# Optimization experiments

Hardware: AMD Instinct MI355X
Metric: run time of the kernel (lower is better)

## Reference

```python
import jax, jax.numpy as jnp
import numpy as np

B, S, D, N = 4, 4096, 512, 512  # d_state must equal d_model for the original broadcast to be valid


def setup_inputs() -> dict:
    key = jax.random.key(0)
    ks = jax.random.split(key, 8)
    inv = 1.0 / np.sqrt(D)
    return {
        "x": jax.random.normal(ks[0], (B, S, D), dtype=jnp.float32),
        "state0": jnp.zeros((B, N), dtype=jnp.float32),
        "W_gate": (jax.random.normal(ks[1], (D, D)) * inv).astype(jnp.float32),  # x_proj_gate.weight [out,in]
        "b_gate": jnp.zeros((D,), jnp.float32),
        "W_sp": (jax.random.normal(ks[2], (N, D)) * inv).astype(jnp.float32),    # state_proj.weight [d_state, d_model]
        "b_sp": jnp.zeros((N,), jnp.float32),
        "W_out": (jax.random.normal(ks[3], (D, D)) * inv).astype(jnp.float32),   # out_proj.weight
        "b_out": jnp.zeros((D,), jnp.float32),
        "A_log": (jax.random.normal(ks[4], (D, N)) * 0.02).astype(jnp.float32),
        "D_param": jnp.ones((D,), jnp.float32),
    }


def reference(x, state0, W_gate, b_gate, W_sp, b_sp, W_out, b_out, A_log, D_param):
    # x_gate = silu(x_proj_gate(x))  [B,S,D]
    x_gate = jax.nn.silu(x @ W_gate.T + b_gate)
    # s = state_proj(x_gate)  [B,S,N]
    s = x_gate @ W_sp.T + b_sp
    # A = -exp(A_log); per-step decay = exp(mean_N(A))  [D] (== N by construction)
    A = -jnp.exp(A_log)
    decay = jnp.exp(A.mean(axis=-1))

    def step(state, s_t):  # state [B,N], s_t [B,N]
        state = state * decay + s_t
        return state, state

    state_f, states = jax.lax.scan(step, state0, jnp.swapaxes(s, 0, 1))  # states [S,B,N]
    # y_t = state_t @ state_proj.weight + D * u_t
    y = jnp.einsum('sbn,nd->bsd', states, W_sp) + D_param * x_gate
    out = y @ W_out.T + b_out  # out_proj
    return out, state_f
```

## Files before the change

### kernel.cpp

```cpp
#include <hip/hip_runtime.h>
#include <hip/hip_bf16.h>
#include <stdint.h>


typedef __bf16 bf16_t;
typedef bf16_t bf16x8 __attribute__((ext_vector_type(8)));
typedef bf16_t bf16x4 __attribute__((ext_vector_type(4)));
typedef float  f32x4  __attribute__((ext_vector_type(4)));

static __device__ __forceinline__ void async_copy16(bf16_t* lds, const bf16_t* g) {
    __builtin_amdgcn_global_load_lds((const __attribute__((address_space(1))) void*)g,
                                     (__attribute__((address_space(3))) void*)lds, 16, 0, 0);
}

template <int MODE, int NT, bool SCAN, bool F32A>
static __device__ __forceinline__ void gemm_body(
    int bid, int nwg, bf16_t* __restrict__ AsB, bf16_t* __restrict__ BsB,
    const void* __restrict__ A0v, const bf16_t* __restrict__ W0,
    const bf16_t* __restrict__ A1, const bf16_t* __restrict__ W1,
    const float* __restrict__ bias, void* __restrict__ outp,
    const float* __restrict__ decay_g, float* __restrict__ carry_g)
{
    constexpr int K = 512;
    const int tid = threadIdx.x;
    if ((nwg & 7) == 0) bid = (bid & 7) * (nwg >> 3) + (bid >> 3);
    const int m0 = (bid >> 2) << 7, n0 = (bid & 3) << 7;
    const int l = tid & 63, w = tid >> 6;
    const int wr = w >> 2, wc = w & 3;
    const int lr = l & 15, kc = l >> 4;
    const int rloc = l >> 3, sc = (l & 7) ^ rloc;

    float bv[2];
    #pragma unroll
    for (int j = 0; j < 2; ++j)
        bv[j] = bias ? bias[n0 + wc * 32 + j * 16 + lr] : 0.f;

    f32x4 acc[4][2];
    const f32x4 z = {0.f, 0.f, 0.f, 0.f};
    #pragma unroll
    for (int i = 0; i < 4; ++i)
        #pragma unroll
        for (int j = 0; j < 2; ++j) acc[i][j] = z;

    const bf16_t* __restrict__ A0b = (const bf16_t*)A0v;
    const float*  __restrict__ A0f = (const float*)A0v;
    const int arow = tid >> 2, aq = tid & 3;

    auto stage = [&](int t) {
        const bf16_t* __restrict__ Asrc = (t < 8) ? A0b : A1;
        const bf16_t* __restrict__ Wsrc = (t < 8) ? W0 : W1;
        const int kk = (t & 7) << 6;
        bf16_t* bufA = AsB + (t & 1) * 8192;
        bf16_t* bufB = BsB + (t & 1) * 8192;
        #pragma unroll
        for (int v = 0; v < 2; ++v) {
            const int win = w * 2 + v;
            async_copy16(bufA + win * 512,
                         Asrc + (size_t)(m0 + win * 8 + rloc) * K + kk + sc * 8);
            async_copy16(bufB + win * 512,
                         Wsrc + (size_t)(n0 + win * 8 + rloc) * K + kk + sc * 8);
        }
    };
    auto stageB = [&](int t) {
        const int kk = (t & 7) << 6;
        bf16_t* bufB = BsB + (t & 1) * 8192;
        #pragma unroll
        for (int v = 0; v < 2; ++v) {
            const int win = w * 2 + v;
            async_copy16(bufB + win * 512,
                         W0 + (size_t)(n0 + win * 8 + rloc) * K + kk + sc * 8);
        }
    };
    float4 arA[4];
    auto issueA = [&](int t) {
        const float* p = A0f + (size_t)(m0 + arow) * K + ((t & 7) << 6) + aq * 16;
        arA[0] = ((const float4*)p)[0];
        arA[1] = ((const float4*)p)[1];
        arA[2] = ((const float4*)p)[2];
        arA[3] = ((const float4*)p)[3];
    };
    auto writeA = [&](int t) {
        bf16x8 v0, v1;
        v0[0]=(bf16_t)arA[0].x; v0[1]=(bf16_t)arA[0].y; v0[2]=(bf16_t)arA[0].z; v0[3]=(bf16_t)arA[0].w;
        v0[4]=(bf16_t)arA[1].x; v0[5]=(bf16_t)arA[1].y; v0[6]=(bf16_t)arA[1].z; v0[7]=(bf16_t)arA[1].w;
        v1[0]=(bf16_t)arA[2].x; v1[1]=(bf16_t)arA[2].y; v1[2]=(bf16_t)arA[2].z; v1[3]=(bf16_t)arA[2].w;
        v1[4]=(bf16_t)arA[3].x; v1[5]=(bf16_t)arA[3].y; v1[6]=(bf16_t)arA[3].z; v1[7]=(bf16_t)arA[3].w;
        bf16_t* bufA = AsB + (t & 1) * 8192;
        *(bf16x8*)(bufA + arow * 64 + (((aq * 2    ) ^ (arow & 7)) << 3)) = v0;
        *(bf16x8*)(bufA + arow * 64 + (((aq * 2 + 1) ^ (arow & 7)) << 3)) = v1;
    };

    if (F32A) { issueA(0); asm volatile("" ::: "memory"); stageB(0); }
    else      { stage(0); }

    #pragma unroll
    for (int t = 0; t < NT; ++t) {
        if (F32A) {
            asm volatile("s_waitcnt vmcnt(2)" ::: "memory");
            writeA(t);
            if (t + 1 < NT) {
                issueA(t + 1);
                asm volatile("" ::: "memory");
                stageB(t + 1);
                asm volatile("s_waitcnt vmcnt(6) lgkmcnt(0)" ::: "memory");
            } else {
                asm volatile("s_waitcnt vmcnt(0) lgkmcnt(0)" ::: "memory");
            }
        } else {
            if (t + 1 < NT) {
                stage(t + 1);
                asm volatile("s_waitcnt vmcnt(4)" ::: "memory");
            } else {
                asm volatile("s_waitcnt vmcnt(0)" ::: "memory");
            }
        }
        __builtin_amdgcn_s_barrier();
        const bf16_t* __restrict__ bufA = AsB + (t & 1) * 8192;
        const bf16_t* __restrict__ bufB = BsB + (t & 1) * 8192;
        bf16x8 a[2][4], b[2][2];
        #pragma unroll
        for (int ks = 0; ks < 2; ++ks) {
            #pragma unroll
            for (int i = 0; i < 4; ++i)
                a[ks][i] = *(const bf16x8*)(bufA + (wr * 64 + i * 16 + lr) * 64
                                            + (((ks * 4 + kc) ^ (lr & 7)) << 3));
            #pragma unroll
            for (int j = 0; j < 2; ++j)
                b[ks][j] = *(const bf16x8*)(bufB + (wc * 32 + j * 16 + lr) * 64
                                            + (((ks * 4 + kc) ^ (lr & 7)) << 3));
        }
        #pragma unroll
        for (int ks = 0; ks < 2; ++ks)
            #pragma unroll
            for (int i = 0; i < 4; ++i)
                #pragma unroll
                for (int j = 0; j < 2; ++j)
                    acc[i][j] = __builtin_amdgcn_mfma_f32_16x16x32_bf16(
                        a[ks][i], b[ks][j], acc[i][j], 0, 0, 0);
        if (t + 1 < NT)
            __builtin_amdgcn_s_barrier();
    }

    if (MODE == 0) {
        float* outF = (float*)outp;
        #pragma unroll
        for (int i = 0; i < 4; ++i) {
            const int row = m0 + wr * 64 + i * 16 + kc * 4;
            #pragma unroll
            for (int j = 0; j < 2; ++j) {
                const int col = n0 + wc * 32 + j * 16 + lr;
                #pragma unroll
                for (int r = 0; r < 4; ++r)
                    outF[(size_t)(row + r) * 512 + col] = acc[i][j][r] + bv[j];
            }
        }
    } else {
        __syncthreads();
        bf16_t* eps = AsB;
        #pragma unroll
        for (int i = 0; i < 4; ++i) {
            const int row = wr * 64 + i * 16 + kc * 4;
            #pragma unroll
            for (int j = 0; j < 2; ++j) {
                const int col = wc * 32 + j * 16 + lr;
                #pragma unroll
                for (int r = 0; r < 4; ++r) {
                    float v = acc[i][j][r] + bv[j];
                    if (MODE == 2) v = v / (1.f + __expf(-v));
                    eps[(row + r) * 128 + col] = (bf16_t)v;
                }
            }
        }
        __syncthreads();
        bf16_t* outB = (bf16_t*)outp;
        #pragma unroll
        for (int s2 = 0; s2 < 4; ++s2) {
            const int row = s2 * 32 + (tid >> 4);
            const int col = (tid & 15) * 8;
            *(bf16x8*)(outB + (size_t)(m0 + row) * 512 + n0 + col) =
                *(const bf16x8*)(eps + row * 128 + col);
        }
        if (SCAN) {
            const int sub = tid >> 7, col = tid & 127;
            const int n = n0 + col;
            const float dec = decay_g[n];
            float st = 0.f;
            #pragma unroll 8
            for (int i = 0; i < 32; ++i)
                st = st * dec + (float)eps[(sub * 32 + i) * 128 + col];
            carry_g[(size_t)((m0 >> 5) + sub) * 512 + n] = st;
        }
    }
}

template <int MODE, int NT, bool SCAN, bool F32A>
__global__ __launch_bounds__(512, 4) void gemm_std(
    const void* __restrict__ A0v, const bf16_t* __restrict__ W0,
    const bf16_t* __restrict__ A1, const bf16_t* __restrict__ W1,
    const float* __restrict__ bias, void* __restrict__ outp,
    const float* __restrict__ decay_g, float* __restrict__ carry_g)
{
    __shared__ bf16_t As[2 * 128 * 64];
    __shared__ bf16_t Bs[2 * 128 * 64];
    gemm_body<MODE, NT, SCAN, F32A>(blockIdx.x, gridDim.x, As, Bs,
                                    A0v, W0, A1, W1, bias, outp, decay_g, carry_g);
}

__global__ __launch_bounds__(512, 4) void g1_wct(
    const float* __restrict__ x, const bf16_t* __restrict__ Wg,
    const float* __restrict__ b_gate, bf16_t* __restrict__ xg,
    const bf16_t* __restrict__ Wo, const bf16_t* __restrict__ Wsp,
    bf16_t* __restrict__ WcT)
{
    __shared__ bf16_t As[2 * 128 * 64];
    __shared__ bf16_t Bs[2 * 128 * 64];
    if (blockIdx.x < 512)
        gemm_body<2, 8, false, true>(blockIdx.x, 512, As, Bs,
            (const void*)x, Wg, (const bf16_t*)nullptr, (const bf16_t*)nullptr,
            b_gate, (void*)xg, (const float*)nullptr, (float*)nullptr);
    else
        gemm_body<1, 8, false, false>(blockIdx.x - 512, 16, As, Bs,
            (const void*)Wo, Wsp, (const bf16_t*)nullptr, (const bf16_t*)nullptr,
            (const float*)nullptr, (void*)WcT, (const float*)nullptr, (float*)nullptr);
}

__global__ void prep_all(const float* __restrict__ Wg, const float* __restrict__ Wsp,
                         const float* __restrict__ Wo, const float* __restrict__ Dp,
                         bf16_t* __restrict__ Wg_bf, bf16_t* __restrict__ Wsp_bf,
                         bf16_t* __restrict__ Wo_bf, bf16_t* __restrict__ W2_bf,
                         const float* __restrict__ A_log, float* __restrict__ decay)
{
    const int blk = blockIdx.x, tid = threadIdx.x;
    {
        int i = blk * 256 + tid;
        Wg_bf[i]  = (bf16_t)Wg[i];
        Wsp_bf[i] = (bf16_t)Wsp[i];
        float wo  = Wo[i];
        Wo_bf[i]  = (bf16_t)wo;
        W2_bf[i]  = (bf16_t)(wo * Dp[i & 511]);
    }
    if (blk < 128) {
        int d = blk * 4 + (tid >> 6);
        int ll = tid & 63;
        const float* row = A_log + (size_t)d * 512;
        float s = 0.f;
        for (int k = ll; k < 512; k += 64) s += expf(row[k]);
        #pragma unroll
        for (int off = 32; off > 0; off >>= 1) s += __shfl_down(s, off);
        if (ll == 0) decay[d] = expf(-s * (1.f / 512.f));
    }
}

__global__ void scan_carry(float* __restrict__ carry, const float* __restrict__ decay,
                           const float* __restrict__ state0, float* __restrict__ state_f)
{
    int g = blockIdx.x * 256 + threadIdx.x;
    int n = g & 511, b = g >> 9;
    float dec = decay[n];
    float d32 = dec;
    #pragma unroll
    for (int t = 0; t < 5; ++t) d32 *= d32;
    float st = state0[g];
    for (int ch = 0; ch < 128; ++ch) {
        size_t idx = (size_t)(b * 128 + ch) * 512 + n;
        float c = carry[idx];
        carry[idx] = st;
        st = st * d32 + c;
    }
    state_f[g] = st;
}

__global__ void scan_final8(const bf16_t* __restrict__ s, const float* __restrict__ decay,
                            const float* __restrict__ exc, bf16_t* __restrict__ states)
{
    int g = blockIdx.x * 128 + threadIdx.x;
    int ng = g & 63, ch = (g >> 6) & 127, b = g >> 13;
    const int n0 = ng * 8;
    float4 d0 = *(const float4*)(decay + n0);
    float4 d1 = *(const float4*)(decay + n0 + 4);
    const float* ep = exc + (size_t)(b * 128 + ch) * 512 + n0;
    float4 s0 = *(const float4*)ep;
    float4 s1 = *(const float4*)(ep + 4);
    float st[8] = {s0.x, s0.y, s0.z, s0.w, s1.x, s1.y, s1.z, s1.w};
    const float dc[8] = {d0.x, d0.y, d0.z, d0.w, d1.x, d1.y, d1.z, d1.w};
    size_t base = (size_t)(b * 4096 + ch * 32) * 512 + n0;
    #pragma unroll 8
    for (int i = 0; i < 32; ++i) {
        bf16x8 v = *(const bf16x8*)(s + base + (size_t)i * 512);
        bf16x8 o;
        #pragma unroll
        for (int k = 0; k < 8; ++k) {
            st[k] = st[k] * dc[k] + (float)v[k];
            o[k] = (bf16_t)st[k];
        }
        *(bf16x8*)(states + base + (size_t)i * 512) = o;
    }
}

extern "C" void kernel_launch(void* const* d_in, const int* in_sizes, int n_in,
                              void* d_out, int out_size, void* d_ws, size_t ws_size,
                              hipStream_t stream)
{
    const float* x      = (const float*)d_in[0];
    const float* state0 = (const float*)d_in[1];
    const float* W_gate = (const float*)d_in[2];
    const float* b_gate = (const float*)d_in[3];
    const float* W_sp   = (const float*)d_in[4];
    const float* b_sp   = (const float*)d_in[5];
    const float* W_out  = (const float*)d_in[6];
    const float* b_out  = (const float*)d_in[7];
    const float* A_log  = (const float*)d_in[8];
    const float* D_par  = (const float*)d_in[9];
    float* out = (float*)d_out;

    char* ws = (char*)d_ws;
    bf16_t* states = (bf16_t*)ws;
    bf16_t* xg_bf  = (bf16_t*)(ws + (16u << 20));
    bf16_t* s_bf   = (bf16_t*)(ws + (32u << 20));
    bf16_t* Wg_bf  = (bf16_t*)(ws + (48u << 20));
    bf16_t* Wsp_bf = Wg_bf + 262144;
    bf16_t* Wo_bf  = Wg_bf + 2 * 262144;
    bf16_t* W2_bf  = Wg_bf + 3 * 262144;
    bf16_t* WcT_bf = Wg_bf + 4 * 262144;
    float*  carry  = (float*)(Wg_bf + 5 * 262144);
    float*  decay  = carry + 262144;

    prep_all<<<dim3(1024), dim3(256), 0, stream>>>(
        W_gate, W_sp, W_out, D_par, Wg_bf, Wsp_bf, Wo_bf, W2_bf, A_log, decay);

    g1_wct<<<dim3(528), dim3(512), 0, stream>>>(
        x, Wg_bf, b_gate, xg_bf, Wo_bf, Wsp_bf, WcT_bf);

    gemm_std<1, 8, true, false><<<dim3(512), dim3(512), 0, stream>>>(
        (const void*)xg_bf, Wsp_bf, (const bf16_t*)nullptr, (const bf16_t*)nullptr,
        b_sp, (void*)s_bf, decay, carry);

    scan_carry<<<dim3(8), dim3(256), 0, stream>>>(carry, decay, state0, out + 8388608);
    scan_final8<<<dim3(256), dim3(128), 0, stream>>>(s_bf, decay, carry, states);

    gemm_std<0, 16, false, false><<<dim3(512), dim3(512), 0, stream>>>(
        (const void*)states, WcT_bf, xg_bf, W2_bf, b_out, (void*)out,
        (const float*)nullptr, (float*)nullptr);
}
```

Baseline: 83.44 us.

## Deepen GEMM shared-memory pipeline to triple buffering with prefetch distance two

Switches the LDS A/B tiles from double to triple buffering and issues global loads two k-tiles ahead instead of one, with the vmcnt waits adjusted to match. For the fp32-A path it double-buffers the register staging of x. The aim is to hide more global memory latency behind the MFMA work. In exchange LDS per block rises from 64KB to 96KB and the launch bound drops from 4 to 2 blocks per CU, which lowers occupancy and adds register pressure.

```diff
diff --git a/kernel.cpp b/kernel.cpp
--- a/kernel.cpp
+++ b/kernel.cpp
@@ -50,8 +50,8 @@
         const bf16_t* __restrict__ Asrc = (t < 8) ? A0b : A1;
         const bf16_t* __restrict__ Wsrc = (t < 8) ? W0 : W1;
         const int kk = (t & 7) << 6;
-        bf16_t* bufA = AsB + (t & 1) * 8192;
-        bf16_t* bufB = BsB + (t & 1) * 8192;
+        bf16_t* bufA = AsB + (t % 3) * 8192;
+        bf16_t* bufB = BsB + (t % 3) * 8192;
         #pragma unroll
         for (int v = 0; v < 2; ++v) {
             const int win = w * 2 + v;
@@ -63,7 +63,7 @@
     };
     auto stageB = [&](int t) {
         const int kk = (t & 7) << 6;
-        bf16_t* bufB = BsB + (t & 1) * 8192;
+        bf16_t* bufB = BsB + (t % 3) * 8192;
         #pragma unroll
         for (int v = 0; v < 2; ++v) {
             const int win = w * 2 + v;
@@ -71,52 +71,51 @@
                          W0 + (size_t)(n0 + win * 8 + rloc) * K + kk + sc * 8);
         }
     };
-    float4 arA[4];
+    float4 arA[2][4];
     auto issueA = [&](int t) {
         const float* p = A0f + (size_t)(m0 + arow) * K + ((t & 7) << 6) + aq * 16;
-        arA[0] = ((const float4*)p)[0];
-        arA[1] = ((const float4*)p)[1];
-        arA[2] = ((const float4*)p)[2];
-        arA[3] = ((const float4*)p)[3];
+        arA[t & 1][0] = ((const float4*)p)[0];
+        arA[t & 1][1] = ((const float4*)p)[1];
+        arA[t & 1][2] = ((const float4*)p)[2];
+        arA[t & 1][3] = ((const float4*)p)[3];
     };
     auto writeA = [&](int t) {
+        const float4* ar = arA[t & 1];
         bf16x8 v0, v1;
-        v0[0]=(bf16_t)arA[0].x; v0[1]=(bf16_t)arA[0].y; v0[2]=(bf16_t)arA[0].z; v0[3]=(bf16_t)arA[0].w;
-        v0[4]=(bf16_t)arA[1].x; v0[5]=(bf16_t)arA[1].y; v0[6]=(bf16_t)arA[1].z; v0[7]=(bf16_t)arA[1].w;
-        v1[0]=(bf16_t)arA[2].x; v1[1]=(bf16_t)arA[2].y; v1[2]=(bf16_t)arA[2].z; v1[3]=(bf16_t)arA[2].w;
-        v1[4]=(bf16_t)arA[3].x; v1[5]=(bf16_t)arA[3].y; v1[6]=(bf16_t)arA[3].z; v1[7]=(bf16_t)arA[3].w;
-        bf16_t* bufA = AsB + (t & 1) * 8192;
+        v0[0]=(bf16_t)ar[0].x; v0[1]=(bf16_t)ar[0].y; v0[2]=(bf16_t)ar[0].z; v0[3]=(bf16_t)ar[0].w;
+        v0[4]=(bf16_t)ar[1].x; v0[5]=(bf16_t)ar[1].y; v0[6]=(bf16_t)ar[1].z; v0[7]=(bf16_t)ar[1].w;
+        v1[0]=(bf16_t)ar[2].x; v1[1]=(bf16_t)ar[2].y; v1[2]=(bf16_t)ar[2].z; v1[3]=(bf16_t)ar[2].w;
+        v1[4]=(bf16_t)ar[3].x; v1[5]=(bf16_t)ar[3].y; v1[6]=(bf16_t)ar[3].z; v1[7]=(bf16_t)ar[3].w;
+        bf16_t* bufA = AsB + (t % 3) * 8192;
         *(bf16x8*)(bufA + arow * 64 + (((aq * 2    ) ^ (arow & 7)) << 3)) = v0;
         *(bf16x8*)(bufA + arow * 64 + (((aq * 2 + 1) ^ (arow & 7)) << 3)) = v1;
     };
 
-    if (F32A) { issueA(0); asm volatile("" ::: "memory"); stageB(0); }
-    else      { stage(0); }
+    if (F32A) { issueA(0); asm volatile("" ::: "memory"); stageB(0);
+                issueA(1); asm volatile("" ::: "memory"); stageB(1); }
+    else      { stage(0); stage(1); }
 
     #pragma unroll
     for (int t = 0; t < NT; ++t) {
         if (F32A) {
-            asm volatile("s_waitcnt vmcnt(2)" ::: "memory");
+            if (t + 1 < NT) asm volatile("s_waitcnt vmcnt(6)" ::: "memory");
+            else            asm volatile("s_waitcnt vmcnt(0)" ::: "memory");
             writeA(t);
-            if (t + 1 < NT) {
-                issueA(t + 1);
+            if (t + 2 < NT) {
+                issueA(t + 2);
                 asm volatile("" ::: "memory");
-                stageB(t + 1);
-                asm volatile("s_waitcnt vmcnt(6) lgkmcnt(0)" ::: "memory");
-            } else {
-                asm volatile("s_waitcnt vmcnt(0) lgkmcnt(0)" ::: "memory");
+                stageB(t + 2);
             }
+            asm volatile("s_waitcnt lgkmcnt(0)" ::: "memory");
         } else {
-            if (t + 1 < NT) {
-                stage(t + 1);
-                asm volatile("s_waitcnt vmcnt(4)" ::: "memory");
-            } else {
-                asm volatile("s_waitcnt vmcnt(0)" ::: "memory");
-            }
+            if (t + 2 < NT) stage(t + 2);
+            if (t + 2 < NT)      asm volatile("s_waitcnt vmcnt(8)" ::: "memory");
+            else if (t + 1 < NT) asm volatile("s_waitcnt vmcnt(4)" ::: "memory");
+            else                 asm volatile("s_waitcnt vmcnt(0)" ::: "memory");
         }
         __builtin_amdgcn_s_barrier();
-        const bf16_t* __restrict__ bufA = AsB + (t & 1) * 8192;
-        const bf16_t* __restrict__ bufB = BsB + (t & 1) * 8192;
+        const bf16_t* __restrict__ bufA = AsB + (t % 3) * 8192;
+        const bf16_t* __restrict__ bufB = BsB + (t % 3) * 8192;
         bf16x8 a[2][4], b[2][2];
         #pragma unroll
         for (int ks = 0; ks < 2; ++ks) {
@@ -194,26 +193,26 @@
 }
 
 template <int MODE, int NT, bool SCAN, bool F32A>
-__global__ __launch_bounds__(512, 4) void gemm_std(
+__global__ __launch_bounds__(512, 2) void gemm_std(
     const void* __restrict__ A0v, const bf16_t* __restrict__ W0,
     const bf16_t* __restrict__ A1, const bf16_t* __restrict__ W1,
     const float* __restrict__ bias, void* __restrict__ outp,
     const float* __restrict__ decay_g, float* __restrict__ carry_g)
 {
-    __shared__ bf16_t As[2 * 128 * 64];
-    __shared__ bf16_t Bs[2 * 128 * 64];
+    __shared__ bf16_t As[3 * 128 * 64];
+    __shared__ bf16_t Bs[3 * 128 * 64];
     gemm_body<MODE, NT, SCAN, F32A>(blockIdx.x, gridDim.x, As, Bs,
                                     A0v, W0, A1, W1, bias, outp, decay_g, carry_g);
 }
 
-__global__ __launch_bounds__(512, 4) void g1_wct(
+__global__ __launch_bounds__(512, 2) void g1_wct(
     const float* __restrict__ x, const bf16_t* __restrict__ Wg,
     const float* __restrict__ b_gate, bf16_t* __restrict__ xg,
     const bf16_t* __restrict__ Wo, const bf16_t* __restrict__ Wsp,
     bf16_t* __restrict__ WcT)
 {
-    __shared__ bf16_t As[2 * 128 * 64];
-    __shared__ bf16_t Bs[2 * 128 * 64];
+    __shared__ bf16_t As[3 * 128 * 64];
+    __shared__ bf16_t Bs[3 * 128 * 64];
     if (blockIdx.x < 512)
         gemm_body<2, 8, false, true>(blockIdx.x, 512, As, Bs,
             (const void*)x, Wg, (const bf16_t*)nullptr, (const bf16_t*)nullptr,
```

Measured after the change: 102.2 us. 1.22x slower.
